# Performance work log

Measured on AMD Instinct MI355X. Metric: run time of the kernel, lower is better.

Reference implementation:

```python
import jax, jax.numpy as jnp
import numpy as np

N = 100_000      # nodes
E = 800_000      # edges per edge type
T = 3            # num_edge_types - 1 relation-specific convs
D_IN = 128
D_OUT = 128


def setup_inputs() -> dict:
    key = jax.random.key(0)
    k1, k2, k3, k4 = jax.random.split(key, 4)
    x = jax.random.normal(k1, (N, D_IN), dtype=jnp.float32)
    edges = jax.random.randint(k2, (T, 2, E), 0, N, dtype=jnp.int32)
    W = jax.random.normal(k3, (T, D_IN, D_OUT), dtype=jnp.float32) * (1.0 / np.sqrt(D_IN))
    b = jax.random.normal(k4, (T, D_OUT), dtype=jnp.float32) * 0.02
    return {"x": x, "edges": edges, "W": W, "b": b}


def _gcn_conv(x, ei, W, b):
    """PyG GCNConv: add self-loops, symmetric D^-1/2 (A+I) D^-1/2 norm, XW, +b."""
    n = x.shape[0]
    xw = x @ W                                   # [N, D_OUT]
    loop = jnp.arange(n, dtype=ei.dtype)
    src = jnp.concatenate([ei[0], loop])         # [E+N]
    dst = jnp.concatenate([ei[1], loop])         # [E+N]
    deg = jax.ops.segment_sum(jnp.ones(src.shape[0], xw.dtype), dst, num_segments=n)
    dis = jnp.where(deg > 0, jax.lax.rsqrt(jnp.maximum(deg, 1e-12)), 0.0)
    norm = dis[src] * dis[dst]                   # [E+N]
    msg = xw[src] * norm[:, None]                # gather-transform: [E+N, D_OUT]
    out = jax.ops.segment_sum(msg, dst, num_segments=n)  # scatter-add back to nodes
    return out + b


def reference(x, edges, W, b):
    # Sum of per-edge-type GCN convolutions into a shared output buffer.
    out = jnp.zeros((x.shape[0], W.shape[-1]), dtype=x.dtype)
    for i in range(edges.shape[0]):              # small fixed relation loop
        out = out + _gcn_conv(x, edges[i], W[i], b[i])
    return out
```

## Files before the change

kernel.cpp:

```cpp
#include <hip/hip_runtime.h>

#define NN 100000
#define EE 800000
#define TT 3
#define D  128
#define NB 391
#define CAPB 7168
#define CHUNK 8192
#define LSTRIDE 392
#define ENC 32767.0f

typedef unsigned short bf16_t;

typedef __bf16 bf16x8_t __attribute__((ext_vector_type(8)));
typedef float  f32x4_t  __attribute__((ext_vector_type(4)));

union ABFrag { bf16x8_t v; uint4 q; };

__device__ __forceinline__ bf16_t f2bf(float f) {
    unsigned u = __float_as_uint(f);
    u += 0x7fff + ((u >> 16) & 1);
    return (bf16_t)(u >> 16);
}
__device__ __forceinline__ float bf_lo(unsigned p) { return __uint_as_float(p << 16); }
__device__ __forceinline__ float bf_hi(unsigned p) { return __uint_as_float(p & 0xFFFF0000u); }

__global__ void quant_kernel(const float* __restrict__ x, bf16_t* __restrict__ xq) {
    int i = (blockIdx.x * 256 + threadIdx.x) * 4;
    if (i >= NN * D) return;
    float4 f = *(const float4*)(x + i);
    uint2 p;
    p.x = (unsigned)f2bf(f.x) | ((unsigned)f2bf(f.y) << 16);
    p.y = (unsigned)f2bf(f.z) | ((unsigned)f2bf(f.w) << 16);
    *(uint2*)(xq + i) = p;
}

__global__ void wconv_kernel(const float* __restrict__ W, bf16_t* __restrict__ WT) {
    int t = blockIdx.y, n = blockIdx.x, k = threadIdx.x;
    WT[((size_t)t * D + n) * D + k] = f2bf(W[((size_t)t * D + k) * D + n]);
}

__global__ __launch_bounds__(512, 8) void bin_kernel(const int* __restrict__ edges,
                                                     int* __restrict__ bcnt,
                                                     unsigned* __restrict__ bin) {
    __shared__ int hist[NB];
    __shared__ int lbase[NB];
    __shared__ int gbase[NB];
    __shared__ int scn[512];
    __shared__ unsigned srec[CHUNK];
    int tid = threadIdx.x;
    int t = blockIdx.y;
    int f0 = blockIdx.x * CHUNK;
    const int* sb = edges + (size_t)t * 2 * EE;
    const int* db = sb + EE;

    for (int i = tid; i < NB; i += 512) hist[i] = 0;
    __syncthreads();

    int4 s4[4], d4[4];
    int rnk[16];
    bool have[4];
#pragma unroll
    for (int j = 0; j < 4; ++j) {
        int e = f0 + ((j * 512 + tid) << 2);
        have[j] = (e < EE);
        if (have[j]) { s4[j] = *(const int4*)(sb + e); d4[j] = *(const int4*)(db + e); }
    }
#pragma unroll
    for (int j = 0; j < 4; ++j) {
        if (have[j]) {
            rnk[j * 4 + 0] = atomicAdd(&hist[d4[j].x >> 8], 1);
            rnk[j * 4 + 1] = atomicAdd(&hist[d4[j].y >> 8], 1);
            rnk[j * 4 + 2] = atomicAdd(&hist[d4[j].z >> 8], 1);
            rnk[j * 4 + 3] = atomicAdd(&hist[d4[j].w >> 8], 1);
        }
    }
    __syncthreads();

    int hv = (tid < NB) ? hist[tid] : 0;
    scn[tid] = hv;
    __syncthreads();
    for (int off = 1; off < 512; off <<= 1) {
        int u = 0;
        if (tid >= off) u = scn[tid - off];
        __syncthreads();
        if (tid >= off) scn[tid] += u;
        __syncthreads();
    }
    if (tid < NB) {
        lbase[tid] = scn[tid] - hv;
        gbase[tid] = (hv > 0) ? atomicAdd(&bcnt[tid], hv) : 0;
    }
    __syncthreads();

#pragma unroll
    for (int j = 0; j < 4; ++j) {
        if (have[j]) {
            int ss[4] = {s4[j].x, s4[j].y, s4[j].z, s4[j].w};
            int dd[4] = {d4[j].x, d4[j].y, d4[j].z, d4[j].w};
#pragma unroll
            for (int k = 0; k < 4; ++k) {
                int bkt = dd[k] >> 8;
                int pos = lbase[bkt] + rnk[j * 4 + k];
                srec[pos] = ((unsigned)(dd[k] & 255) << 19) | ((unsigned)t << 17) | (unsigned)ss[k];
            }
        }
    }
    __syncthreads();

    int nval = EE - f0; if (nval > CHUNK) nval = CHUNK;
    for (int i = tid; i < nval; i += 512) {
        int lo = 0;
#pragma unroll
        for (int step = 256; step > 0; step >>= 1) {
            int cand = lo + step;
            if (cand < NB && lbase[cand] <= i) lo = cand;
        }
        int rel = gbase[lo] + (i - lbase[lo]);
        if (rel < CAPB) bin[(size_t)lo * CAPB + rel] = srec[i];
    }
}

#define MAXR 14
__global__ __launch_bounds__(512) void sort_kernel(const int* __restrict__ bcnt,
                                                   unsigned* __restrict__ bin,
                                                   float* __restrict__ dis3,
                                                   int* __restrict__ cnts3,
                                                   int* __restrict__ nodeoff) {
    __shared__ int cnt[768];
    __shared__ int tot[256];
    int tid = threadIdx.x;
    int b = blockIdx.x;
    int c = bcnt[b]; if (c > CAPB) c = CAPB;
    unsigned* reg = bin + (size_t)b * CAPB;

    for (int i = tid; i < 768; i += 512) cnt[i] = 0;
    __syncthreads();

    unsigned ur[MAXR];
    int rr[MAXR];
    bool vld[MAXR];
#pragma unroll
    for (int k = 0; k < MAXR; ++k) {
        int i = tid + k * 512;
        vld[k] = (i < c);
        unsigned u = vld[k] ? reg[i] : 0u;
        ur[k] = u;
        int bi = (int)(u >> 19) * 3 + (int)((u >> 17) & 3);
        rr[k] = vld[k] ? atomicAdd(&cnt[bi], 1) : 0;
    }
    __syncthreads();

    int d0 = 0, d1 = 0, d2 = 0;
    if (tid < 256) {
        d0 = cnt[tid * 3]; d1 = cnt[tid * 3 + 1]; d2 = cnt[tid * 3 + 2];
        tot[tid] = d0 + d1 + d2;
    }
    __syncthreads();
    for (int off = 1; off < 256; off <<= 1) {
        int v = 0;
        if (tid < 256 && tid >= off) v = tot[tid - off];
        __syncthreads();
        if (tid < 256 && tid >= off) tot[tid] += v;
        __syncthreads();
    }
    if (tid < 256) {
        int excl = tot[tid] - (d0 + d1 + d2);
        int gnode = b * 256 + tid;
        if (gnode < NN) {
            nodeoff[gnode] = b * CAPB + excl;
            cnts3[gnode]   = d0 | (d1 << 8) | (d2 << 16);
            dis3[gnode]            = rsqrtf((float)d0 + 1.f);
            dis3[NN + gnode]       = rsqrtf((float)d1 + 1.f);
            dis3[2 * NN + gnode]   = rsqrtf((float)d2 + 1.f);
        }
        cnt[tid * 3]     = excl;
        cnt[tid * 3 + 1] = excl + d0;
        cnt[tid * 3 + 2] = excl + d0 + d1;
    }
    __syncthreads();
#pragma unroll
    for (int k = 0; k < MAXR; ++k) {
        if (vld[k]) {
            unsigned u = ur[k];
            int bi = (int)(u >> 19) * 3 + (int)((u >> 17) & 3);
            reg[cnt[bi] + rr[k]] = u & 0x1FFFFu;
        }
    }
}


#define ISSUE(UX, SA, UW, J0)                                                      \
    {                                                                              \
        const int _j0 = (J0);                                                      \
        _Pragma("unroll")                                                          \
        for (int k = 0; k < 8; ++k) {                                              \
            SA[k] = __builtin_amdgcn_readlane((int)(UW), _j0 + k);                 \
            int sxk = SA[k] & 0x1FFFF;                                             \
            UX[k] = *(const unsigned*)(xq + (size_t)sxk * D + (lane << 1));        \
        }                                                                          \
    }

#define CONSUME(UX, SA, J0, B1, B2, A00, A01, A10, A11, A20, A21)                  \
    {                                                                              \
        const int _j0 = (J0);                                                      \
        _Pragma("unroll")                                                          \
        for (int k = 0; k < 8; ++k) {                                              \
            int idxk = _j0 + k;                                                    \
            float wk = (float)(((unsigned)SA[k]) >> 17);                           \
            unsigned u = UX[k];                                                    \
            float xl = bf_lo(u), xh = bf_hi(u);                                    \
            if (idxk < B1)      { A00 += wk * xl; A01 += wk * xh; }                \
            else if (idxk < B2) { A10 += wk * xl; A11 += wk * xh; }                \
            else                { A20 += wk * xl; A21 += wk * xh; }                \
        }                                                                          \
    }

__global__ __launch_bounds__(512, 8) void fused_kernel(const bf16_t* __restrict__ xq,
                                                       const float* __restrict__ dis3,
                                                       const int* __restrict__ cnts3,
                                                       const int* __restrict__ nodeoff,
                                                       const unsigned* __restrict__ recs,
                                                       const bf16_t* __restrict__ WT,
                                                       const float* __restrict__ bias,
                                                       float* __restrict__ out) {
    __shared__ __attribute__((aligned(16))) ushort ylds[16 * LSTRIDE];
    int tid  = threadIdx.x;
    int lane = tid & 63;
    int wave = tid >> 6;
    int n0 = blockIdx.x * 16;
    int nA = n0 + wave * 2;
    int nB = nA + 1;

    unsigned suA = *(const unsigned*)(xq + (size_t)nA * D + (lane << 1));
    unsigned suB = *(const unsigned*)(xq + (size_t)nB * D + (lane << 1));
    int pkA = cnts3[nA], pkB = cnts3[nB];
    int s0A = nodeoff[nA], s0B = nodeoff[nB];

    int dA0 = pkA & 255, dA1 = (pkA >> 8) & 255, dA2 = (pkA >> 16) & 255;
    int dB0 = pkB & 255, dB1 = (pkB >> 8) & 255, dB2 = (pkB >> 16) & 255;
    float dnA0 = rsqrtf((float)dA0 + 1.f), dnA1 = rsqrtf((float)dA1 + 1.f),
          dnA2 = rsqrtf((float)dA2 + 1.f);
    float dnB0 = rsqrtf((float)dB0 + 1.f), dnB1 = rsqrtf((float)dB1 + 1.f),
          dnB2 = rsqrtf((float)dB2 + 1.f);

    int b1A = __builtin_amdgcn_readfirstlane(dA0);
    int b2A = __builtin_amdgcn_readfirstlane(dA0 + dA1);
    int cTA = dA0 + dA1 + dA2; if (cTA > 64) cTA = 64;
    int cSA = __builtin_amdgcn_readfirstlane(cTA);
    int b1B = __builtin_amdgcn_readfirstlane(dB0);
    int b2B = __builtin_amdgcn_readfirstlane(dB0 + dB1);
    int cTB = dB0 + dB1 + dB2; if (cTB > 64) cTB = 64;
    int cSB = __builtin_amdgcn_readfirstlane(cTB);

    unsigned urA = recs[s0A + lane];
    unsigned urB = recs[s0B + lane];
    int tlA = (lane < b1A) ? 0 : (lane < b2A) ? 1 : 2;
    int tlB = (lane < b1B) ? 0 : (lane < b2B) ? 1 : 2;
    int vsA = (int)(urA & 0x1FFFFu); if (vsA >= NN) vsA = 0;
    int vsB = (int)(urB & 0x1FFFFu); if (vsB >= NN) vsB = 0;
    float wsA = (lane < cSA) ? dis3[tlA * NN + vsA] : 0.0f;
    float wsB = (lane < cSB) ? dis3[tlB * NN + vsB] : 0.0f;
    unsigned uwA = ((unsigned)(wsA * ENC + 0.5f) << 17) | (unsigned)vsA;
    unsigned uwB = ((unsigned)(wsB * ENC + 0.5f) << 17) | (unsigned)vsB;

    float xsA0 = bf_lo(suA), xsA1 = bf_hi(suA);
    float xsB0 = bf_lo(suB), xsB1 = bf_hi(suB);

    float aA00 = dnA0 * ENC * xsA0, aA01 = dnA0 * ENC * xsA1;
    float aA10 = dnA1 * ENC * xsA0, aA11 = dnA1 * ENC * xsA1;
    float aA20 = dnA2 * ENC * xsA0, aA21 = dnA2 * ENC * xsA1;
    float aB00 = dnB0 * ENC * xsB0, aB01 = dnB0 * ENC * xsB1;
    float aB10 = dnB1 * ENC * xsB0, aB11 = dnB1 * ENC * xsB1;
    float aB20 = dnB2 * ENC * xsB0, aB21 = dnB2 * ENC * xsB1;

    unsigned uxA[8], uxB[8];
    int sA[8], sB[8];

    int nbA = (cSA + 7) >> 3;
    int nbB = (cSB + 7) >> 3;
    if (nbA > 0) ISSUE(uxA, sA, uwA, 0)
    if (nbB > 0) ISSUE(uxB, sB, uwB, 0)
    int nbmax = nbA > nbB ? nbA : nbB;
    for (int blk = 0; blk < nbmax; ++blk) {
        if (blk < nbA) {
            CONSUME(uxA, sA, blk * 8, b1A, b2A, aA00, aA01, aA10, aA11, aA20, aA21)
            if (blk + 1 < nbA) ISSUE(uxA, sA, uwA, (blk + 1) * 8)
        }
        if (blk < nbB) {
            CONSUME(uxB, sB, blk * 8, b1B, b2B, aB00, aB01, aB10, aB11, aB20, aB21)
            if (blk + 1 < nbB) ISSUE(uxB, sB, uwB, (blk + 1) * 8)
        }
    }

    {
        float fA0 = dnA0 * (1.0f / ENC), fA1 = dnA1 * (1.0f / ENC), fA2 = dnA2 * (1.0f / ENC);
        float fB0 = dnB0 * (1.0f / ENC), fB1 = dnB1 * (1.0f / ENC), fB2 = dnB2 * (1.0f / ENC);
        ushort* ywA = ylds + (wave * 2) * LSTRIDE + (lane << 1);
        ushort* ywB = ywA + LSTRIDE;
        *(unsigned*)(ywA)         = (unsigned)f2bf(aA00 * fA0) | ((unsigned)f2bf(aA01 * fA0) << 16);
        *(unsigned*)(ywA + D)     = (unsigned)f2bf(aA10 * fA1) | ((unsigned)f2bf(aA11 * fA1) << 16);
        *(unsigned*)(ywA + 2 * D) = (unsigned)f2bf(aA20 * fA2) | ((unsigned)f2bf(aA21 * fA2) << 16);
        *(unsigned*)(ywB)         = (unsigned)f2bf(aB00 * fB0) | ((unsigned)f2bf(aB01 * fB0) << 16);
        *(unsigned*)(ywB + D)     = (unsigned)f2bf(aB10 * fB1) | ((unsigned)f2bf(aB11 * fB1) << 16);
        *(unsigned*)(ywB + 2 * D) = (unsigned)f2bf(aB20 * fB2) | ((unsigned)f2bf(aB21 * fB2) << 16);
    }
    __syncthreads();

    {
        int quad = lane >> 4;
        int lid  = lane & 15;
        int col  = wave * 16 + lid;
        f32x4_t acc = {0.f, 0.f, 0.f, 0.f};
        const ushort* yr = ylds + lid * LSTRIDE;
#pragma unroll
        for (int t = 0; t < TT; ++t) {
            const bf16_t* wn = WT + ((size_t)t * D + col) * D;
#pragma unroll
            for (int s = 0; s < 4; ++s) {
                ABFrag av, bv;
                av.q = *(const uint4*)(yr + t * D + s * 32 + quad * 8);
                bv.q = *(const uint4*)(wn + s * 32 + quad * 8);
                acc = __builtin_amdgcn_mfma_f32_16x16x32_bf16(av.v, bv.v, acc, 0, 0, 0);
            }
        }
        float bc = bias[col] + bias[D + col] + bias[2 * D + col];
#pragma unroll
        for (int r = 0; r < 4; ++r)
            out[(size_t)(n0 + quad * 4 + r) * D + col] = acc[r] + bc;
    }
}

extern "C" void kernel_launch(void* const* d_in, const int* in_sizes, int n_in,
                              void* d_out, int out_size, void* d_ws, size_t ws_size,
                              hipStream_t stream) {
    const float* x     = (const float*)d_in[0];
    const int*   edges = (const int*)d_in[1];
    const float* W     = (const float*)d_in[2];
    const float* b     = (const float*)d_in[3];
    float*       out   = (float*)d_out;

    char* w = (char*)d_ws;
    bf16_t*   xq      = (bf16_t*)w;
    unsigned* bin     = (unsigned*)(w + (size_t)NN * D * 2);
    float*    dis3    = (float*)((char*)bin + (size_t)NB * CAPB * 4);
    int*      cnts3   = (int*)((char*)dis3 + (size_t)3 * NN * 4);
    int*      nodeoff = cnts3 + NN;
    bf16_t*   WT      = (bf16_t*)(nodeoff + NN);
    int*      bcnt    = (int*)((char*)WT + (size_t)TT * D * D * 2);

    hipMemsetAsync(bcnt, 0, (size_t)NB * sizeof(int), stream);

    quant_kernel<<<(NN * D / 4 + 255) / 256, 256, 0, stream>>>(x, xq);
    {
        dim3 g(D, TT);
        wconv_kernel<<<g, D, 0, stream>>>(W, WT);
    }

    {
        dim3 g((EE + CHUNK - 1) / CHUNK, TT);
        bin_kernel<<<g, 512, 0, stream>>>(edges, bcnt, bin);
    }

    sort_kernel<<<NB, 512, 0, stream>>>(bcnt, bin, dis3, cnts3, nodeoff);

    fused_kernel<<<NN / 16, 512, 0, stream>>>(xq, dis3, cnts3, nodeoff, bin, WT, b, out);
}
```

Baseline: 309.3 us.

## Fuse per-bin sort into aggregation kernel using LDS-resident sorted edge records

The per-bin counting sort no longer writes sorted records back to global memory. A light count kernel now only computes degrees and dis3, and it also absorbs the weight transpose/convert work, which removes the separate wconv launch. The aggregation kernel redoes the sort for half a bin, stages records with precomputed source norms into shared memory, then loops over eight 16-node groups per block. This saves the global write and reread of sorted edges and the separate per-edge dis3 gather. In exchange it re-reads each bin twice, uses much more LDS per block, lowers the occupancy hint and adds serial group iterations per block.

```diff
diff --git a/kernel.cpp b/kernel.cpp
--- a/kernel.cpp
+++ b/kernel.cpp
@@ -9,6 +9,7 @@
 #define CHUNK 8192
 #define LSTRIDE 392
 #define ENC 32767.0f
+#define HCAP 4160
 
 typedef unsigned short bf16_t;
 
@@ -33,11 +34,6 @@
     p.x = (unsigned)f2bf(f.x) | ((unsigned)f2bf(f.y) << 16);
     p.y = (unsigned)f2bf(f.z) | ((unsigned)f2bf(f.w) << 16);
     *(uint2*)(xq + i) = p;
-}
-
-__global__ void wconv_kernel(const float* __restrict__ W, bf16_t* __restrict__ WT) {
-    int t = blockIdx.y, n = blockIdx.x, k = threadIdx.x;
-    WT[((size_t)t * D + n) * D + k] = f2bf(W[((size_t)t * D + k) * D + n]);
 }
 
 __global__ __launch_bounds__(512, 8) void bin_kernel(const int* __restrict__ edges,
@@ -122,69 +118,42 @@
 }
 
 #define MAXR 14
-__global__ __launch_bounds__(512) void sort_kernel(const int* __restrict__ bcnt,
-                                                   unsigned* __restrict__ bin,
-                                                   float* __restrict__ dis3,
-                                                   int* __restrict__ cnts3,
-                                                   int* __restrict__ nodeoff) {
-    __shared__ int cnt[768];
-    __shared__ int tot[256];
+__global__ __launch_bounds__(512) void count_kernel(const int* __restrict__ bcnt,
+                                                    const unsigned* __restrict__ bin,
+                                                    float* __restrict__ dis3,
+                                                    const float* __restrict__ W,
+                                                    bf16_t* __restrict__ WT) {
     int tid = threadIdx.x;
     int b = blockIdx.x;
+    if (b >= NB) {
+        int t = b - NB;
+        for (int i = tid; i < D * D; i += 512) {
+            int n = i >> 7, k = i & 127;
+            WT[((size_t)t * D + n) * D + k] = f2bf(W[((size_t)t * D + k) * D + n]);
+        }
+        return;
+    }
+    __shared__ int cnt[768];
     int c = bcnt[b]; if (c > CAPB) c = CAPB;
-    unsigned* reg = bin + (size_t)b * CAPB;
+    const unsigned* reg = bin + (size_t)b * CAPB;
 
     for (int i = tid; i < 768; i += 512) cnt[i] = 0;
     __syncthreads();
-
-    unsigned ur[MAXR];
-    int rr[MAXR];
-    bool vld[MAXR];
 #pragma unroll
     for (int k = 0; k < MAXR; ++k) {
         int i = tid + k * 512;
-        vld[k] = (i < c);
-        unsigned u = vld[k] ? reg[i] : 0u;
-        ur[k] = u;
-        int bi = (int)(u >> 19) * 3 + (int)((u >> 17) & 3);
-        rr[k] = vld[k] ? atomicAdd(&cnt[bi], 1) : 0;
-    }
-    __syncthreads();
-
-    int d0 = 0, d1 = 0, d2 = 0;
+        if (i < c) {
+            unsigned u = reg[i];
+            atomicAdd(&cnt[(int)(u >> 19) * 3 + (int)((u >> 17) & 3)], 1);
+        }
+    }
+    __syncthreads();
     if (tid < 256) {
-        d0 = cnt[tid * 3]; d1 = cnt[tid * 3 + 1]; d2 = cnt[tid * 3 + 2];
-        tot[tid] = d0 + d1 + d2;
-    }
-    __syncthreads();
-    for (int off = 1; off < 256; off <<= 1) {
-        int v = 0;
-        if (tid < 256 && tid >= off) v = tot[tid - off];
-        __syncthreads();
-        if (tid < 256 && tid >= off) tot[tid] += v;
-        __syncthreads();
-    }
-    if (tid < 256) {
-        int excl = tot[tid] - (d0 + d1 + d2);
         int gnode = b * 256 + tid;
         if (gnode < NN) {
-            nodeoff[gnode] = b * CAPB + excl;
-            cnts3[gnode]   = d0 | (d1 << 8) | (d2 << 16);
-            dis3[gnode]            = rsqrtf((float)d0 + 1.f);
-            dis3[NN + gnode]       = rsqrtf((float)d1 + 1.f);
-            dis3[2 * NN + gnode]   = rsqrtf((float)d2 + 1.f);
-        }
-        cnt[tid * 3]     = excl;
-        cnt[tid * 3 + 1] = excl + d0;
-        cnt[tid * 3 + 2] = excl + d0 + d1;
-    }
-    __syncthreads();
-#pragma unroll
-    for (int k = 0; k < MAXR; ++k) {
-        if (vld[k]) {
-            unsigned u = ur[k];
-            int bi = (int)(u >> 19) * 3 + (int)((u >> 17) & 3);
-            reg[cnt[bi] + rr[k]] = u & 0x1FFFFu;
+            dis3[gnode]          = rsqrtf((float)cnt[tid * 3] + 1.f);
+            dis3[NN + gnode]     = rsqrtf((float)cnt[tid * 3 + 1] + 1.f);
+            dis3[2 * NN + gnode] = rsqrtf((float)cnt[tid * 3 + 2] + 1.f);
         }
     }
 }
@@ -216,118 +185,187 @@
         }                                                                          \
     }
 
-__global__ __launch_bounds__(512, 8) void fused_kernel(const bf16_t* __restrict__ xq,
-                                                       const float* __restrict__ dis3,
-                                                       const int* __restrict__ cnts3,
-                                                       const int* __restrict__ nodeoff,
-                                                       const unsigned* __restrict__ recs,
-                                                       const bf16_t* __restrict__ WT,
-                                                       const float* __restrict__ bias,
-                                                       float* __restrict__ out) {
+__global__ __launch_bounds__(512, 6) void sortfused_kernel(const bf16_t* __restrict__ xq,
+                                                           const float* __restrict__ dis3,
+                                                           const int* __restrict__ bcnt,
+                                                           const unsigned* __restrict__ bin,
+                                                           const bf16_t* __restrict__ WT,
+                                                           const float* __restrict__ bias,
+                                                           float* __restrict__ out) {
+    __shared__ unsigned srec[HCAP];
     __shared__ __attribute__((aligned(16))) ushort ylds[16 * LSTRIDE];
+    __shared__ int cnt[384];
+    __shared__ int ndoff[128];
+    __shared__ int pkl[128];
+    __shared__ int tot[128];
+
     int tid  = threadIdx.x;
     int lane = tid & 63;
     int wave = tid >> 6;
-    int n0 = blockIdx.x * 16;
-    int nA = n0 + wave * 2;
-    int nB = nA + 1;
-
-    unsigned suA = *(const unsigned*)(xq + (size_t)nA * D + (lane << 1));
-    unsigned suB = *(const unsigned*)(xq + (size_t)nB * D + (lane << 1));
-    int pkA = cnts3[nA], pkB = cnts3[nB];
-    int s0A = nodeoff[nA], s0B = nodeoff[nB];
-
-    int dA0 = pkA & 255, dA1 = (pkA >> 8) & 255, dA2 = (pkA >> 16) & 255;
-    int dB0 = pkB & 255, dB1 = (pkB >> 8) & 255, dB2 = (pkB >> 16) & 255;
-    float dnA0 = rsqrtf((float)dA0 + 1.f), dnA1 = rsqrtf((float)dA1 + 1.f),
-          dnA2 = rsqrtf((float)dA2 + 1.f);
-    float dnB0 = rsqrtf((float)dB0 + 1.f), dnB1 = rsqrtf((float)dB1 + 1.f),
-          dnB2 = rsqrtf((float)dB2 + 1.f);
-
-    int b1A = __builtin_amdgcn_readfirstlane(dA0);
-    int b2A = __builtin_amdgcn_readfirstlane(dA0 + dA1);
-    int cTA = dA0 + dA1 + dA2; if (cTA > 64) cTA = 64;
-    int cSA = __builtin_amdgcn_readfirstlane(cTA);
-    int b1B = __builtin_amdgcn_readfirstlane(dB0);
-    int b2B = __builtin_amdgcn_readfirstlane(dB0 + dB1);
-    int cTB = dB0 + dB1 + dB2; if (cTB > 64) cTB = 64;
-    int cSB = __builtin_amdgcn_readfirstlane(cTB);
-
-    unsigned urA = recs[s0A + lane];
-    unsigned urB = recs[s0B + lane];
-    int tlA = (lane < b1A) ? 0 : (lane < b2A) ? 1 : 2;
-    int tlB = (lane < b1B) ? 0 : (lane < b2B) ? 1 : 2;
-    int vsA = (int)(urA & 0x1FFFFu); if (vsA >= NN) vsA = 0;
-    int vsB = (int)(urB & 0x1FFFFu); if (vsB >= NN) vsB = 0;
-    float wsA = (lane < cSA) ? dis3[tlA * NN + vsA] : 0.0f;
-    float wsB = (lane < cSB) ? dis3[tlB * NN + vsB] : 0.0f;
-    unsigned uwA = ((unsigned)(wsA * ENC + 0.5f) << 17) | (unsigned)vsA;
-    unsigned uwB = ((unsigned)(wsB * ENC + 0.5f) << 17) | (unsigned)vsB;
-
-    float xsA0 = bf_lo(suA), xsA1 = bf_hi(suA);
-    float xsB0 = bf_lo(suB), xsB1 = bf_hi(suB);
-
-    float aA00 = dnA0 * ENC * xsA0, aA01 = dnA0 * ENC * xsA1;
-    float aA10 = dnA1 * ENC * xsA0, aA11 = dnA1 * ENC * xsA1;
-    float aA20 = dnA2 * ENC * xsA0, aA21 = dnA2 * ENC * xsA1;
-    float aB00 = dnB0 * ENC * xsB0, aB01 = dnB0 * ENC * xsB1;
-    float aB10 = dnB1 * ENC * xsB0, aB11 = dnB1 * ENC * xsB1;
-    float aB20 = dnB2 * ENC * xsB0, aB21 = dnB2 * ENC * xsB1;
-
-    unsigned uxA[8], uxB[8];
-    int sA[8], sB[8];
-
-    int nbA = (cSA + 7) >> 3;
-    int nbB = (cSB + 7) >> 3;
-    if (nbA > 0) ISSUE(uxA, sA, uwA, 0)
-    if (nbB > 0) ISSUE(uxB, sB, uwB, 0)
-    int nbmax = nbA > nbB ? nbA : nbB;
-    for (int blk = 0; blk < nbmax; ++blk) {
-        if (blk < nbA) {
-            CONSUME(uxA, sA, blk * 8, b1A, b2A, aA00, aA01, aA10, aA11, aA20, aA21)
-            if (blk + 1 < nbA) ISSUE(uxA, sA, uwA, (blk + 1) * 8)
-        }
-        if (blk < nbB) {
-            CONSUME(uxB, sB, blk * 8, b1B, b2B, aB00, aB01, aB10, aB11, aB20, aB21)
-            if (blk + 1 < nbB) ISSUE(uxB, sB, uwB, (blk + 1) * 8)
-        }
-    }
-
-    {
-        float fA0 = dnA0 * (1.0f / ENC), fA1 = dnA1 * (1.0f / ENC), fA2 = dnA2 * (1.0f / ENC);
-        float fB0 = dnB0 * (1.0f / ENC), fB1 = dnB1 * (1.0f / ENC), fB2 = dnB2 * (1.0f / ENC);
-        ushort* ywA = ylds + (wave * 2) * LSTRIDE + (lane << 1);
-        ushort* ywB = ywA + LSTRIDE;
-        *(unsigned*)(ywA)         = (unsigned)f2bf(aA00 * fA0) | ((unsigned)f2bf(aA01 * fA0) << 16);
-        *(unsigned*)(ywA + D)     = (unsigned)f2bf(aA10 * fA1) | ((unsigned)f2bf(aA11 * fA1) << 16);
-        *(unsigned*)(ywA + 2 * D) = (unsigned)f2bf(aA20 * fA2) | ((unsigned)f2bf(aA21 * fA2) << 16);
-        *(unsigned*)(ywB)         = (unsigned)f2bf(aB00 * fB0) | ((unsigned)f2bf(aB01 * fB0) << 16);
-        *(unsigned*)(ywB + D)     = (unsigned)f2bf(aB10 * fB1) | ((unsigned)f2bf(aB11 * fB1) << 16);
-        *(unsigned*)(ywB + 2 * D) = (unsigned)f2bf(aB20 * fB2) | ((unsigned)f2bf(aB21 * fB2) << 16);
-    }
-    __syncthreads();
-
-    {
-        int quad = lane >> 4;
-        int lid  = lane & 15;
-        int col  = wave * 16 + lid;
-        f32x4_t acc = {0.f, 0.f, 0.f, 0.f};
-        const ushort* yr = ylds + lid * LSTRIDE;
-#pragma unroll
-        for (int t = 0; t < TT; ++t) {
-            const bf16_t* wn = WT + ((size_t)t * D + col) * D;
-#pragma unroll
-            for (int s = 0; s < 4; ++s) {
-                ABFrag av, bv;
-                av.q = *(const uint4*)(yr + t * D + s * 32 + quad * 8);
-                bv.q = *(const uint4*)(wn + s * 32 + quad * 8);
-                acc = __builtin_amdgcn_mfma_f32_16x16x32_bf16(av.v, bv.v, acc, 0, 0, 0);
+    int b    = blockIdx.x >> 1;
+    int half = blockIdx.x & 1;
+    int nbase = b * 256 + half * 128;
+
+    int c = bcnt[b]; if (c > CAPB) c = CAPB;
+    const unsigned* reg = bin + (size_t)b * CAPB;
+
+    for (int i = tid; i < 384; i += 512) cnt[i] = 0;
+    __syncthreads();
+
+    unsigned ur[MAXR];
+    int rr[MAXR];
+    bool vld[MAXR];
+#pragma unroll
+    for (int k = 0; k < MAXR; ++k) {
+        int i = tid + k * 512;
+        bool v = (i < c);
+        unsigned u = v ? reg[i] : 0u;
+        int node8 = (int)(u >> 19);
+        bool mine = v && ((node8 >> 7) == half);
+        ur[k] = u;
+        int bi = (node8 & 127) * 3 + (int)((u >> 17) & 3);
+        rr[k] = mine ? atomicAdd(&cnt[bi], 1) : 0;
+        vld[k] = mine;
+    }
+    __syncthreads();
+
+    int d0 = 0, d1 = 0, d2 = 0;
+    if (tid < 128) {
+        d0 = cnt[tid * 3]; d1 = cnt[tid * 3 + 1]; d2 = cnt[tid * 3 + 2];
+        tot[tid] = d0 + d1 + d2;
+    }
+    __syncthreads();
+    for (int off = 1; off < 128; off <<= 1) {
+        int v = 0;
+        if (tid < 128 && tid >= off) v = tot[tid - off];
+        __syncthreads();
+        if (tid < 128 && tid >= off) tot[tid] += v;
+        __syncthreads();
+    }
+    if (tid < 128) {
+        int excl = tot[tid] - (d0 + d1 + d2);
+        ndoff[tid] = excl;
+        pkl[tid]   = d0 | (d1 << 8) | (d2 << 16);
+        cnt[tid * 3]     = excl;
+        cnt[tid * 3 + 1] = excl + d0;
+        cnt[tid * 3 + 2] = excl + d0 + d1;
+    }
+    __syncthreads();
+
+#pragma unroll
+    for (int k = 0; k < MAXR; ++k) {
+        if (vld[k]) {
+            unsigned u = ur[k];
+            int node8 = (int)(u >> 19);
+            int bi = (node8 & 127) * 3 + (int)((u >> 17) & 3);
+            int pos = cnt[bi] + rr[k];
+            int src = (int)(u & 0x1FFFFu);
+            float w = dis3[((u >> 17) & 3) * NN + src];
+            if (pos < HCAP)
+                srec[pos] = ((unsigned)(w * ENC + 0.5f) << 17) | (unsigned)src;
+        }
+    }
+    __syncthreads();
+
+    int quad  = lane >> 4;
+    int lid16 = lane & 15;
+    int col   = wave * 16 + lid16;
+    float bc = bias[col] + bias[D + col] + bias[2 * D + col];
+
+    for (int g = 0; g < 8; ++g) {
+        int n0g = nbase + g * 16;
+        if (n0g >= NN) break;
+        int lA = g * 16 + wave * 2;
+        int lB = lA + 1;
+        int nA = nbase + lA, nB = nbase + lB;
+
+        int pkA = pkl[lA], pkB = pkl[lB];
+        int offA = ndoff[lA], offB = ndoff[lB];
+
+        unsigned suA = *(const unsigned*)(xq + (size_t)nA * D + (lane << 1));
+        unsigned suB = *(const unsigned*)(xq + (size_t)nB * D + (lane << 1));
+
+        int dA0 = pkA & 255, dA1 = (pkA >> 8) & 255, dA2 = (pkA >> 16) & 255;
+        int dB0 = pkB & 255, dB1 = (pkB >> 8) & 255, dB2 = (pkB >> 16) & 255;
+        float dnA0 = rsqrtf((float)dA0 + 1.f), dnA1 = rsqrtf((float)dA1 + 1.f),
+              dnA2 = rsqrtf((float)dA2 + 1.f);
+        float dnB0 = rsqrtf((float)dB0 + 1.f), dnB1 = rsqrtf((float)dB1 + 1.f),
+              dnB2 = rsqrtf((float)dB2 + 1.f);
+
+        int b1A = __builtin_amdgcn_readfirstlane(dA0);
+        int b2A = __builtin_amdgcn_readfirstlane(dA0 + dA1);
+        int cSA = __builtin_amdgcn_readfirstlane(dA0 + dA1 + dA2);
+        if (cSA > 64) cSA = 64;
+        int b1B = __builtin_amdgcn_readfirstlane(dB0);
+        int b2B = __builtin_amdgcn_readfirstlane(dB0 + dB1);
+        int cSB = __builtin_amdgcn_readfirstlane(dB0 + dB1 + dB2);
+        if (cSB > 64) cSB = 64;
+
+        unsigned uwA = (lane < cSA) ? srec[offA + lane] : 0u;
+        unsigned uwB = (lane < cSB) ? srec[offB + lane] : 0u;
+
+        float xsA0 = bf_lo(suA), xsA1 = bf_hi(suA);
+        float xsB0 = bf_lo(suB), xsB1 = bf_hi(suB);
+
+        float aA00 = dnA0 * ENC * xsA0, aA01 = dnA0 * ENC * xsA1;
+        float aA10 = dnA1 * ENC * xsA0, aA11 = dnA1 * ENC * xsA1;
+        float aA20 = dnA2 * ENC * xsA0, aA21 = dnA2 * ENC * xsA1;
+        float aB00 = dnB0 * ENC * xsB0, aB01 = dnB0 * ENC * xsB1;
+        float aB10 = dnB1 * ENC * xsB0, aB11 = dnB1 * ENC * xsB1;
+        float aB20 = dnB2 * ENC * xsB0, aB21 = dnB2 * ENC * xsB1;
+
+        unsigned uxA[8], uxB[8];
+        int sA[8], sB[8];
+
+        int nbA = (cSA + 7) >> 3;
+        int nbB = (cSB + 7) >> 3;
+        if (nbA > 0) ISSUE(uxA, sA, uwA, 0)
+        if (nbB > 0) ISSUE(uxB, sB, uwB, 0)
+        int nbmax = nbA > nbB ? nbA : nbB;
+        for (int blk = 0; blk < nbmax; ++blk) {
+            if (blk < nbA) {
+                CONSUME(uxA, sA, blk * 8, b1A, b2A, aA00, aA01, aA10, aA11, aA20, aA21)
+                if (blk + 1 < nbA) ISSUE(uxA, sA, uwA, (blk + 1) * 8)
             }
-        }
-        float bc = bias[col] + bias[D + col] + bias[2 * D + col];
-#pragma unroll
-        for (int r = 0; r < 4; ++r)
-            out[(size_t)(n0 + quad * 4 + r) * D + col] = acc[r] + bc;
+            if (blk < nbB) {
+                CONSUME(uxB, sB, blk * 8, b1B, b2B, aB00, aB01, aB10, aB11, aB20, aB21)
+                if (blk + 1 < nbB) ISSUE(uxB, sB, uwB, (blk + 1) * 8)
+            }
+        }
+
+        {
+            float fA0 = dnA0 * (1.0f / ENC), fA1 = dnA1 * (1.0f / ENC), fA2 = dnA2 * (1.0f / ENC);
+            float fB0 = dnB0 * (1.0f / ENC), fB1 = dnB1 * (1.0f / ENC), fB2 = dnB2 * (1.0f / ENC);
+            ushort* ywA = ylds + (wave * 2) * LSTRIDE + (lane << 1);
+            ushort* ywB = ywA + LSTRIDE;
+            *(unsigned*)(ywA)         = (unsigned)f2bf(aA00 * fA0) | ((unsigned)f2bf(aA01 * fA0) << 16);
+            *(unsigned*)(ywA + D)     = (unsigned)f2bf(aA10 * fA1) | ((unsigned)f2bf(aA11 * fA1) << 16);
+            *(unsigned*)(ywA + 2 * D) = (unsigned)f2bf(aA20 * fA2) | ((unsigned)f2bf(aA21 * fA2) << 16);
+            *(unsigned*)(ywB)         = (unsigned)f2bf(aB00 * fB0) | ((unsigned)f2bf(aB01 * fB0) << 16);
+            *(unsigned*)(ywB + D)     = (unsigned)f2bf(aB10 * fB1) | ((unsigned)f2bf(aB11 * fB1) << 16);
+            *(unsigned*)(ywB + 2 * D) = (unsigned)f2bf(aB20 * fB2) | ((unsigned)f2bf(aB21 * fB2) << 16);
+        }
+        __syncthreads();
+
+        {
+            f32x4_t acc = {0.f, 0.f, 0.f, 0.f};
+            const ushort* yr = ylds + lid16 * LSTRIDE;
+#pragma unroll
+            for (int t = 0; t < TT; ++t) {
+                const bf16_t* wn = WT + ((size_t)t * D + col) * D;
+#pragma unroll
+                for (int s = 0; s < 4; ++s) {
+                    ABFrag av, bv;
+                    av.q = *(const uint4*)(yr + t * D + s * 32 + quad * 8);
+                    bv.q = *(const uint4*)(wn + s * 32 + quad * 8);
+                    acc = __builtin_amdgcn_mfma_f32_16x16x32_bf16(av.v, bv.v, acc, 0, 0, 0);
+                }
+            }
+#pragma unroll
+            for (int r = 0; r < 4; ++r)
+                out[(size_t)(n0g + quad * 4 + r) * D + col] = acc[r] + bc;
+        }
+        __syncthreads();
     }
 }
 
@@ -341,28 +379,22 @@
     float*       out   = (float*)d_out;
 
     char* w = (char*)d_ws;
-    bf16_t*   xq      = (bf16_t*)w;
-    unsigned* bin     = (unsigned*)(w + (size_t)NN * D * 2);
-    float*    dis3    = (float*)((char*)bin + (size_t)NB * CAPB * 4);
-    int*      cnts3   = (int*)((char*)dis3 + (size_t)3 * NN * 4);
-    int*      nodeoff = cnts3 + NN;
-    bf16_t*   WT      = (bf16_t*)(nodeoff + NN);
-    int*      bcnt    = (int*)((char*)WT + (size_t)TT * D * D * 2);
+    bf16_t*   xq   = (bf16_t*)w;
+    unsigned* bin  = (unsigned*)(w + (size_t)NN * D * 2);
+    float*    dis3 = (float*)((char*)bin + (size_t)NB * CAPB * 4);
+    bf16_t*   WT   = (bf16_t*)((char*)dis3 + (size_t)3 * NN * 4);
+    int*      bcnt = (int*)((char*)WT + (size_t)TT * D * D * 2);
 
     hipMemsetAsync(bcnt, 0, (size_t)NB * sizeof(int), stream);
 
     quant_kernel<<<(NN * D / 4 + 255) / 256, 256, 0, stream>>>(x, xq);
-    {
-        dim3 g(D, TT);
-        wconv_kernel<<<g, D, 0, stream>>>(W, WT);
-    }
 
     {
         dim3 g((EE + CHUNK - 1) / CHUNK, TT);
         bin_kernel<<<g, 512, 0, stream>>>(edges, bcnt, bin);
     }
 
-    sort_kernel<<<NB, 512, 0, stream>>>(bcnt, bin, dis3, cnts3, nodeoff);
-
-    fused_kernel<<<NN / 16, 512, 0, stream>>>(xq, dis3, cnts3, nodeoff, bin, WT, b, out);
-}
+    count_kernel<<<NB + TT, 512, 0, stream>>>(bcnt, bin, dis3, W, WT);
+
+    sortfused_kernel<<<NB * 2, 512, 0, stream>>>(xq, dis3, bcnt, bin, WT, b, out);
+}
```

After: 366.8 us. 18.6% more time.

## Replace per-bin sort with fixed-capacity slot records carrying precomputed edge weights

Applied to the files above, without the earlier changes.

Splits the old sort kernel in two. A count kernel computes per-node degrees and also absorbs the weight transpose. A slot kernel then writes each edge into a fixed 64-entry per-node slot with the full symmetric norm weight and the edge type packed in. The fused kernel reads records directly, so it no longer needs the extra dis3 gather, the nodeoff lookup or the prefix-scan boundaries. The costs are an extra kernel launch, a second pass over the bins, zero-filling the slot array, a coarser 13-bit weight encoding, and unordered slot placement from atomics.

```diff
diff --git a/kernel.cpp b/kernel.cpp
--- a/kernel.cpp
+++ b/kernel.cpp
@@ -8,7 +8,8 @@
 #define CAPB 7168
 #define CHUNK 8192
 #define LSTRIDE 392
-#define ENC 32767.0f
+#define CAP 64
+#define ENC 8191.0f
 
 typedef unsigned short bf16_t;
 
@@ -33,11 +34,6 @@
     p.x = (unsigned)f2bf(f.x) | ((unsigned)f2bf(f.y) << 16);
     p.y = (unsigned)f2bf(f.z) | ((unsigned)f2bf(f.w) << 16);
     *(uint2*)(xq + i) = p;
-}
-
-__global__ void wconv_kernel(const float* __restrict__ W, bf16_t* __restrict__ WT) {
-    int t = blockIdx.y, n = blockIdx.x, k = threadIdx.x;
-    WT[((size_t)t * D + n) * D + k] = f2bf(W[((size_t)t * D + k) * D + n]);
 }
 
 __global__ __launch_bounds__(512, 8) void bin_kernel(const int* __restrict__ edges,
@@ -122,69 +118,86 @@
 }
 
 #define MAXR 14
-__global__ __launch_bounds__(512) void sort_kernel(const int* __restrict__ bcnt,
-                                                   unsigned* __restrict__ bin,
-                                                   float* __restrict__ dis3,
-                                                   int* __restrict__ cnts3,
-                                                   int* __restrict__ nodeoff) {
+__global__ __launch_bounds__(512) void count_kernel(const int* __restrict__ bcnt,
+                                                    const unsigned* __restrict__ bin,
+                                                    float* __restrict__ dis3,
+                                                    int* __restrict__ cnts3,
+                                                    const float* __restrict__ W,
+                                                    bf16_t* __restrict__ WT) {
+    int tid = threadIdx.x;
+    int b = blockIdx.x;
+    if (b >= NB) {
+        int t = b - NB;
+        for (int i = tid; i < D * D; i += 512) {
+            int n = i >> 7, k = i & 127;
+            WT[((size_t)t * D + n) * D + k] = f2bf(W[((size_t)t * D + k) * D + n]);
+        }
+        return;
+    }
     __shared__ int cnt[768];
-    __shared__ int tot[256];
+    int c = bcnt[b]; if (c > CAPB) c = CAPB;
+    const unsigned* reg = bin + (size_t)b * CAPB;
+
+    for (int i = tid; i < 768; i += 512) cnt[i] = 0;
+    __syncthreads();
+#pragma unroll
+    for (int k = 0; k < MAXR; ++k) {
+        int i = tid + k * 512;
+        if (i < c) {
+            unsigned u = reg[i];
+            atomicAdd(&cnt[(int)(u >> 19) * 3 + (int)((u >> 17) & 3)], 1);
+        }
+    }
+    __syncthreads();
+    if (tid < 256) {
+        int gnode = b * 256 + tid;
+        if (gnode < NN) {
+            int d0 = cnt[tid * 3], d1 = cnt[tid * 3 + 1], d2 = cnt[tid * 3 + 2];
+            cnts3[gnode]         = d0 | (d1 << 8) | (d2 << 16);
+            dis3[gnode]          = rsqrtf((float)d0 + 1.f);
+            dis3[NN + gnode]     = rsqrtf((float)d1 + 1.f);
+            dis3[2 * NN + gnode] = rsqrtf((float)d2 + 1.f);
+        }
+    }
+}
+
+__global__ __launch_bounds__(512) void slot_kernel(const int* __restrict__ bcnt,
+                                                   const unsigned* __restrict__ bin,
+                                                   const float* __restrict__ dis3,
+                                                   const int* __restrict__ cnts3,
+                                                   unsigned* __restrict__ recs) {
+    __shared__ int rkc[256];
+    __shared__ float dnl[3][256];
     int tid = threadIdx.x;
     int b = blockIdx.x;
     int c = bcnt[b]; if (c > CAPB) c = CAPB;
-    unsigned* reg = bin + (size_t)b * CAPB;
-
-    for (int i = tid; i < 768; i += 512) cnt[i] = 0;
-    __syncthreads();
-
-    unsigned ur[MAXR];
-    int rr[MAXR];
-    bool vld[MAXR];
+    const unsigned* reg = bin + (size_t)b * CAPB;
+    unsigned* base = recs + (size_t)b * 256 * CAP;
+
+    if (tid < 256) {
+        int gnode = b * 256 + tid;
+        int pk = (gnode < NN) ? cnts3[gnode] : 0;
+        dnl[0][tid] = rsqrtf((float)(pk & 255) + 1.f);
+        dnl[1][tid] = rsqrtf((float)((pk >> 8) & 255) + 1.f);
+        dnl[2][tid] = rsqrtf((float)((pk >> 16) & 255) + 1.f);
+        rkc[tid] = 0;
+    }
+    for (int i = tid; i < 256 * CAP; i += 512) base[i] = 0u;
+    __syncthreads();
+
 #pragma unroll
     for (int k = 0; k < MAXR; ++k) {
         int i = tid + k * 512;
-        vld[k] = (i < c);
-        unsigned u = vld[k] ? reg[i] : 0u;
-        ur[k] = u;
-        int bi = (int)(u >> 19) * 3 + (int)((u >> 17) & 3);
-        rr[k] = vld[k] ? atomicAdd(&cnt[bi], 1) : 0;
-    }
-    __syncthreads();
-
-    int d0 = 0, d1 = 0, d2 = 0;
-    if (tid < 256) {
-        d0 = cnt[tid * 3]; d1 = cnt[tid * 3 + 1]; d2 = cnt[tid * 3 + 2];
-        tot[tid] = d0 + d1 + d2;
-    }
-    __syncthreads();
-    for (int off = 1; off < 256; off <<= 1) {
-        int v = 0;
-        if (tid < 256 && tid >= off) v = tot[tid - off];
-        __syncthreads();
-        if (tid < 256 && tid >= off) tot[tid] += v;
-        __syncthreads();
-    }
-    if (tid < 256) {
-        int excl = tot[tid] - (d0 + d1 + d2);
-        int gnode = b * 256 + tid;
-        if (gnode < NN) {
-            nodeoff[gnode] = b * CAPB + excl;
-            cnts3[gnode]   = d0 | (d1 << 8) | (d2 << 16);
-            dis3[gnode]            = rsqrtf((float)d0 + 1.f);
-            dis3[NN + gnode]       = rsqrtf((float)d1 + 1.f);
-            dis3[2 * NN + gnode]   = rsqrtf((float)d2 + 1.f);
-        }
-        cnt[tid * 3]     = excl;
-        cnt[tid * 3 + 1] = excl + d0;
-        cnt[tid * 3 + 2] = excl + d0 + d1;
-    }
-    __syncthreads();
-#pragma unroll
-    for (int k = 0; k < MAXR; ++k) {
-        if (vld[k]) {
-            unsigned u = ur[k];
-            int bi = (int)(u >> 19) * 3 + (int)((u >> 17) & 3);
-            reg[cnt[bi] + rr[k]] = u & 0x1FFFFu;
+        if (i < c) {
+            unsigned u = reg[i];
+            int node8 = (int)(u >> 19);
+            int t = (int)((u >> 17) & 3);
+            int src = (int)(u & 0x1FFFFu);
+            float w = dis3[t * NN + src] * dnl[t][node8];
+            int r = atomicAdd(&rkc[node8], 1);
+            if (r < CAP)
+                base[node8 * CAP + r] =
+                    ((unsigned)(w * ENC + 0.5f) << 19) | ((unsigned)t << 17) | (unsigned)src;
         }
     }
 }
@@ -201,25 +214,23 @@
         }                                                                          \
     }
 
-#define CONSUME(UX, SA, J0, B1, B2, A00, A01, A10, A11, A20, A21)                  \
+#define CONSUME(UX, SA, A00, A01, A10, A11, A20, A21)                              \
     {                                                                              \
-        const int _j0 = (J0);                                                      \
         _Pragma("unroll")                                                          \
         for (int k = 0; k < 8; ++k) {                                              \
-            int idxk = _j0 + k;                                                    \
-            float wk = (float)(((unsigned)SA[k]) >> 17);                           \
+            unsigned sa = (unsigned)SA[k];                                         \
+            float wk = (float)(sa >> 19);                                          \
+            int tk = (int)((sa >> 17) & 3);                                        \
             unsigned u = UX[k];                                                    \
             float xl = bf_lo(u), xh = bf_hi(u);                                    \
-            if (idxk < B1)      { A00 += wk * xl; A01 += wk * xh; }                \
-            else if (idxk < B2) { A10 += wk * xl; A11 += wk * xh; }                \
-            else                { A20 += wk * xl; A21 += wk * xh; }                \
+            if (tk == 0)      { A00 += wk * xl; A01 += wk * xh; }                  \
+            else if (tk == 1) { A10 += wk * xl; A11 += wk * xh; }                  \
+            else              { A20 += wk * xl; A21 += wk * xh; }                  \
         }                                                                          \
     }
 
 __global__ __launch_bounds__(512, 8) void fused_kernel(const bf16_t* __restrict__ xq,
-                                                       const float* __restrict__ dis3,
                                                        const int* __restrict__ cnts3,
-                                                       const int* __restrict__ nodeoff,
                                                        const unsigned* __restrict__ recs,
                                                        const bf16_t* __restrict__ WT,
                                                        const float* __restrict__ bias,
@@ -232,10 +243,11 @@
     int nA = n0 + wave * 2;
     int nB = nA + 1;
 
+    unsigned uwA = recs[(size_t)nA * CAP + lane];
+    unsigned uwB = recs[(size_t)nB * CAP + lane];
     unsigned suA = *(const unsigned*)(xq + (size_t)nA * D + (lane << 1));
     unsigned suB = *(const unsigned*)(xq + (size_t)nB * D + (lane << 1));
     int pkA = cnts3[nA], pkB = cnts3[nB];
-    int s0A = nodeoff[nA], s0B = nodeoff[nB];
 
     int dA0 = pkA & 255, dA1 = (pkA >> 8) & 255, dA2 = (pkA >> 16) & 255;
     int dB0 = pkB & 255, dB1 = (pkB >> 8) & 255, dB2 = (pkB >> 16) & 255;
@@ -243,36 +255,20 @@
           dnA2 = rsqrtf((float)dA2 + 1.f);
     float dnB0 = rsqrtf((float)dB0 + 1.f), dnB1 = rsqrtf((float)dB1 + 1.f),
           dnB2 = rsqrtf((float)dB2 + 1.f);
-
-    int b1A = __builtin_amdgcn_readfirstlane(dA0);
-    int b2A = __builtin_amdgcn_readfirstlane(dA0 + dA1);
-    int cTA = dA0 + dA1 + dA2; if (cTA > 64) cTA = 64;
+    int cTA = dA0 + dA1 + dA2; if (cTA > CAP) cTA = CAP;
+    int cTB = dB0 + dB1 + dB2; if (cTB > CAP) cTB = CAP;
     int cSA = __builtin_amdgcn_readfirstlane(cTA);
-    int b1B = __builtin_amdgcn_readfirstlane(dB0);
-    int b2B = __builtin_amdgcn_readfirstlane(dB0 + dB1);
-    int cTB = dB0 + dB1 + dB2; if (cTB > 64) cTB = 64;
     int cSB = __builtin_amdgcn_readfirstlane(cTB);
-
-    unsigned urA = recs[s0A + lane];
-    unsigned urB = recs[s0B + lane];
-    int tlA = (lane < b1A) ? 0 : (lane < b2A) ? 1 : 2;
-    int tlB = (lane < b1B) ? 0 : (lane < b2B) ? 1 : 2;
-    int vsA = (int)(urA & 0x1FFFFu); if (vsA >= NN) vsA = 0;
-    int vsB = (int)(urB & 0x1FFFFu); if (vsB >= NN) vsB = 0;
-    float wsA = (lane < cSA) ? dis3[tlA * NN + vsA] : 0.0f;
-    float wsB = (lane < cSB) ? dis3[tlB * NN + vsB] : 0.0f;
-    unsigned uwA = ((unsigned)(wsA * ENC + 0.5f) << 17) | (unsigned)vsA;
-    unsigned uwB = ((unsigned)(wsB * ENC + 0.5f) << 17) | (unsigned)vsB;
 
     float xsA0 = bf_lo(suA), xsA1 = bf_hi(suA);
     float xsB0 = bf_lo(suB), xsB1 = bf_hi(suB);
 
-    float aA00 = dnA0 * ENC * xsA0, aA01 = dnA0 * ENC * xsA1;
-    float aA10 = dnA1 * ENC * xsA0, aA11 = dnA1 * ENC * xsA1;
-    float aA20 = dnA2 * ENC * xsA0, aA21 = dnA2 * ENC * xsA1;
-    float aB00 = dnB0 * ENC * xsB0, aB01 = dnB0 * ENC * xsB1;
-    float aB10 = dnB1 * ENC * xsB0, aB11 = dnB1 * ENC * xsB1;
-    float aB20 = dnB2 * ENC * xsB0, aB21 = dnB2 * ENC * xsB1;
+    float aA00 = dnA0 * dnA0 * ENC * xsA0, aA01 = dnA0 * dnA0 * ENC * xsA1;
+    float aA10 = dnA1 * dnA1 * ENC * xsA0, aA11 = dnA1 * dnA1 * ENC * xsA1;
+    float aA20 = dnA2 * dnA2 * ENC * xsA0, aA21 = dnA2 * dnA2 * ENC * xsA1;
+    float aB00 = dnB0 * dnB0 * ENC * xsB0, aB01 = dnB0 * dnB0 * ENC * xsB1;
+    float aB10 = dnB1 * dnB1 * ENC * xsB0, aB11 = dnB1 * dnB1 * ENC * xsB1;
+    float aB20 = dnB2 * dnB2 * ENC * xsB0, aB21 = dnB2 * dnB2 * ENC * xsB1;
 
     unsigned uxA[8], uxB[8];
     int sA[8], sB[8];
@@ -284,26 +280,25 @@
     int nbmax = nbA > nbB ? nbA : nbB;
     for (int blk = 0; blk < nbmax; ++blk) {
         if (blk < nbA) {
-            CONSUME(uxA, sA, blk * 8, b1A, b2A, aA00, aA01, aA10, aA11, aA20, aA21)
+            CONSUME(uxA, sA, aA00, aA01, aA10, aA11, aA20, aA21)
             if (blk + 1 < nbA) ISSUE(uxA, sA, uwA, (blk + 1) * 8)
         }
         if (blk < nbB) {
-            CONSUME(uxB, sB, blk * 8, b1B, b2B, aB00, aB01, aB10, aB11, aB20, aB21)
+            CONSUME(uxB, sB, aB00, aB01, aB10, aB11, aB20, aB21)
             if (blk + 1 < nbB) ISSUE(uxB, sB, uwB, (blk + 1) * 8)
         }
     }
 
     {
-        float fA0 = dnA0 * (1.0f / ENC), fA1 = dnA1 * (1.0f / ENC), fA2 = dnA2 * (1.0f / ENC);
-        float fB0 = dnB0 * (1.0f / ENC), fB1 = dnB1 * (1.0f / ENC), fB2 = dnB2 * (1.0f / ENC);
+        const float fs = 1.0f / ENC;
         ushort* ywA = ylds + (wave * 2) * LSTRIDE + (lane << 1);
         ushort* ywB = ywA + LSTRIDE;
-        *(unsigned*)(ywA)         = (unsigned)f2bf(aA00 * fA0) | ((unsigned)f2bf(aA01 * fA0) << 16);
-        *(unsigned*)(ywA + D)     = (unsigned)f2bf(aA10 * fA1) | ((unsigned)f2bf(aA11 * fA1) << 16);
-        *(unsigned*)(ywA + 2 * D) = (unsigned)f2bf(aA20 * fA2) | ((unsigned)f2bf(aA21 * fA2) << 16);
-        *(unsigned*)(ywB)         = (unsigned)f2bf(aB00 * fB0) | ((unsigned)f2bf(aB01 * fB0) << 16);
-        *(unsigned*)(ywB + D)     = (unsigned)f2bf(aB10 * fB1) | ((unsigned)f2bf(aB11 * fB1) << 16);
-        *(unsigned*)(ywB + 2 * D) = (unsigned)f2bf(aB20 * fB2) | ((unsigned)f2bf(aB21 * fB2) << 16);
+        *(unsigned*)(ywA)         = (unsigned)f2bf(aA00 * fs) | ((unsigned)f2bf(aA01 * fs) << 16);
+        *(unsigned*)(ywA + D)     = (unsigned)f2bf(aA10 * fs) | ((unsigned)f2bf(aA11 * fs) << 16);
+        *(unsigned*)(ywA + 2 * D) = (unsigned)f2bf(aA20 * fs) | ((unsigned)f2bf(aA21 * fs) << 16);
+        *(unsigned*)(ywB)         = (unsigned)f2bf(aB00 * fs) | ((unsigned)f2bf(aB01 * fs) << 16);
+        *(unsigned*)(ywB + D)     = (unsigned)f2bf(aB10 * fs) | ((unsigned)f2bf(aB11 * fs) << 16);
+        *(unsigned*)(ywB + 2 * D) = (unsigned)f2bf(aB20 * fs) | ((unsigned)f2bf(aB21 * fs) << 16);
     }
     __syncthreads();
 
@@ -341,28 +336,26 @@
     float*       out   = (float*)d_out;
 
     char* w = (char*)d_ws;
-    bf16_t*   xq      = (bf16_t*)w;
-    unsigned* bin     = (unsigned*)(w + (size_t)NN * D * 2);
-    float*    dis3    = (float*)((char*)bin + (size_t)NB * CAPB * 4);
-    int*      cnts3   = (int*)((char*)dis3 + (size_t)3 * NN * 4);
-    int*      nodeoff = cnts3 + NN;
-    bf16_t*   WT      = (bf16_t*)(nodeoff + NN);
-    int*      bcnt    = (int*)((char*)WT + (size_t)TT * D * D * 2);
+    bf16_t*   xq    = (bf16_t*)w;
+    unsigned* bin   = (unsigned*)(w + (size_t)NN * D * 2);
+    unsigned* recs  = (unsigned*)((char*)bin + (size_t)NB * CAPB * 4);
+    float*    dis3  = (float*)((char*)recs + (size_t)NB * 256 * CAP * 4);
+    int*      cnts3 = (int*)((char*)dis3 + (size_t)3 * NN * 4);
+    bf16_t*   WT    = (bf16_t*)(cnts3 + NN);
+    int*      bcnt  = (int*)((char*)WT + (size_t)TT * D * D * 2);
 
     hipMemsetAsync(bcnt, 0, (size_t)NB * sizeof(int), stream);
 
     quant_kernel<<<(NN * D / 4 + 255) / 256, 256, 0, stream>>>(x, xq);
-    {
-        dim3 g(D, TT);
-        wconv_kernel<<<g, D, 0, stream>>>(W, WT);
-    }
 
     {
         dim3 g((EE + CHUNK - 1) / CHUNK, TT);
         bin_kernel<<<g, 512, 0, stream>>>(edges, bcnt, bin);
     }
 
-    sort_kernel<<<NB, 512, 0, stream>>>(bcnt, bin, dis3, cnts3, nodeoff);
-
-    fused_kernel<<<NN / 16, 512, 0, stream>>>(xq, dis3, cnts3, nodeoff, bin, WT, b, out);
-}
+    count_kernel<<<NB + TT, 512, 0, stream>>>(bcnt, bin, dis3, cnts3, W, WT);
+
+    slot_kernel<<<NB, 512, 0, stream>>>(bcnt, bin, dis3, cnts3, recs);
+
+    fused_kernel<<<NN / 16, 512, 0, stream>>>(xq, cnts3, recs, WT, b, out);
+}
```

Measured after the change: 318.3 us. +2.9%, slower.
